# Kernel tuning notes

Measured on AMD Instinct MI355X. Metric: run time of the kernel, lower is better.

Reference implementation:

```python
import jax, jax.numpy as jnp
import numpy as np


def setup_inputs() -> dict:
    key = jax.random.key(0)
    k1, k2 = jax.random.split(key)
    video_feat = jax.random.normal(k1, (64, 1024, 512), dtype=jnp.float32)
    lang_feat = jax.random.normal(k2, (64, 512, 512), dtype=jnp.float32)
    return {"video_feat": video_feat, "lang_feat": lang_feat}


def _batch_pairwise_dist(x, y):
    # x: [B, Nv, D], y: [B, Nl, D] -> [B, Nv, Nl] squared-L2 (expanded form)
    a = jnp.sum(x * x, axis=2, keepdims=True)            # [B, Nv, 1]
    b = jnp.sum(y * y, axis=2, keepdims=True)            # [B, Nl, 1]
    ab = jnp.einsum('bvd,bld->bvl', x, y)                # [B, Nv, Nl]
    return a - 2.0 * ab + jnp.swapaxes(b, 1, 2)


def reference(video_feat, lang_feat):
    pairwise_dist = _batch_pairwise_dist(video_feat, lang_feat)  # [B, Nv, Nl]
    Nv = pairwise_dist.shape[1]
    Nl = pairwise_dist.shape[2]
    language_to_clip_dist = jnp.min(pairwise_dist, axis=2).sum(axis=1) / Nv
    clip_to_language_dist = jnp.min(pairwise_dist, axis=1).sum(axis=1) / Nl
    return language_to_clip_dist + clip_to_language_dist  # [B]
```

## Files before the change

kernel.cpp:

```cpp
#include <hip/hip_runtime.h>
#include <math.h>

#define BATCH 64
#define NV 1024
#define NL 512
#define DIM 512
#define TMM 256
#define TNN 256
#define BK 32
#define NKT (DIM / BK)

typedef __bf16 bf16x8 __attribute__((ext_vector_type(8)));
typedef __bf16 bf16x4 __attribute__((ext_vector_type(4)));
typedef float f32x4 __attribute__((ext_vector_type(4)));

__global__ __launch_bounds__(512, 2) void fused_distmin_kernel(
    const float* __restrict__ video, const float* __restrict__ lang,
    float* __restrict__ rowpart, float* __restrict__ colpart) {
    __shared__ __align__(16) ushort AsU[2][4][TMM][8];
    __shared__ __align__(16) ushort BsU[2][4][TNN][8];
    __shared__ float anrm[TMM], bnrm[TNN];
    float* rowred = (float*)AsU;
    float* colred = (float*)AsU + 2 * TMM;

    const int wg = ((blockIdx.x & 7) << 6) | (blockIdx.x >> 3);
    const int b = wg >> 3;
    const int mt = (wg >> 1) & 3;
    const int nt = wg & 1;

    const int tid = threadIdx.x;
    const int lane = tid & 63;
    const int w = tid >> 6;
    const int wrow = w >> 1;
    const int wcol = w & 1;
    const int lr = lane & 15;
    const int g = lane >> 4;

    const int half = tid & 1;
    const int o_sl = (tid >> 4) & 3;
    const int srow = ((tid >> 6) << 3) + ((tid >> 1) & 7);
    const int skq = o_sl * 2 + half;

    const float* Ath = video + ((size_t)b * NV + (size_t)mt * TMM + srow) * DIM + skq * 4;
    const float* Bth = lang + ((size_t)b * NL + (size_t)nt * TNN + srow) * DIM + skq * 4;

    float nA[4] = {0.f, 0.f, 0.f, 0.f};
    float nB[4] = {0.f, 0.f, 0.f, 0.f};

    f32x4 acc[4][8];
#pragma unroll
    for (int i = 0; i < 4; i++)
#pragma unroll
        for (int j = 0; j < 8; j++) acc[i][j] = (f32x4){0.f, 0.f, 0.f, 0.f};

    float4 va[4], vb[4];

    auto load_chunk = [&](int k0) {
#pragma unroll
        for (int t = 0; t < 4; ++t) {
            va[t] = *(const float4*)(Ath + (size_t)t * 64 * DIM + k0);
            vb[t] = *(const float4*)(Bth + (size_t)t * 64 * DIM + k0);
        }
    };
    auto write_chunk = [&](int buf) {
#pragma unroll
        for (int t = 0; t < 4; ++t) {
            float4 v = va[t];
            nA[t] += v.x * v.x + v.y * v.y + v.z * v.z + v.w * v.w;
            bf16x4 p = {(__bf16)v.x, (__bf16)v.y, (__bf16)v.z, (__bf16)v.w};
            *(bf16x4*)&AsU[buf][o_sl][srow + 64 * t][half * 4] = p;
            float4 u = vb[t];
            nB[t] += u.x * u.x + u.y * u.y + u.z * u.z + u.w * u.w;
            bf16x4 q = {(__bf16)u.x, (__bf16)u.y, (__bf16)u.z, (__bf16)u.w};
            *(bf16x4*)&BsU[buf][o_sl][srow + 64 * t][half * 4] = q;
        }
    };

    load_chunk(0);
    write_chunk(0);
    __syncthreads();

    for (int kt = 0; kt < NKT; ++kt) {
        const int cur = kt & 1;
        const bool more = (kt + 1) < NKT;
        if (more) load_chunk((kt + 1) * BK);

        bf16x8 av[4], bv[8];
#pragma unroll
        for (int fr = 0; fr < 4; ++fr)
            av[fr] = *(const bf16x8*)&AsU[cur][g][wrow * 64 + fr * 16 + lr][0];
#pragma unroll
        for (int fc = 0; fc < 8; ++fc)
            bv[fc] = *(const bf16x8*)&BsU[cur][g][wcol * 128 + fc * 16 + lr][0];
#pragma unroll
        for (int fr = 0; fr < 4; ++fr)
#pragma unroll
            for (int fc = 0; fc < 8; ++fc)
                acc[fr][fc] = __builtin_amdgcn_mfma_f32_16x16x32_bf16(
                    av[fr], bv[fc], acc[fr][fc], 0, 0, 0);

        if (more) write_chunk(cur ^ 1);
        __syncthreads();
    }

#pragma unroll
    for (int si = 0; si < 3; ++si) {
        const int s = (si == 0) ? 1 : (si == 1) ? 16 : 32;
#pragma unroll
        for (int t = 0; t < 4; ++t) {
            nA[t] += __shfl_xor(nA[t], s);
            nB[t] += __shfl_xor(nB[t], s);
        }
    }
    if ((tid & 49) == 0) {
#pragma unroll
        for (int t = 0; t < 4; ++t) {
            anrm[srow + 64 * t] = nA[t];
            bnrm[srow + 64 * t] = nB[t];
        }
    }
    __syncthreads();

    const int rgrp = (lane >> 4) * 4;
    float anorm[4][4];
#pragma unroll
    for (int fr = 0; fr < 4; ++fr)
#pragma unroll
        for (int r = 0; r < 4; ++r)
            anorm[fr][r] = anrm[wrow * 64 + fr * 16 + rgrp + r];
    float bnorm[8];
#pragma unroll
    for (int fc = 0; fc < 8; ++fc)
        bnorm[fc] = bnrm[wcol * 128 + fc * 16 + lr];

    float rmin[4][4];
    float cmin[8];
#pragma unroll
    for (int fr = 0; fr < 4; ++fr)
#pragma unroll
        for (int r = 0; r < 4; ++r) rmin[fr][r] = INFINITY;
#pragma unroll
    for (int fc = 0; fc < 8; ++fc) cmin[fc] = INFINITY;

#pragma unroll
    for (int fr = 0; fr < 4; ++fr)
#pragma unroll
        for (int fc = 0; fc < 8; ++fc)
#pragma unroll
            for (int r = 0; r < 4; ++r) {
                float d = anorm[fr][r] - 2.0f * acc[fr][fc][r] + bnorm[fc];
                rmin[fr][r] = fminf(rmin[fr][r], d);
                cmin[fc] = fminf(cmin[fc], d);
            }

#pragma unroll
    for (int fr = 0; fr < 4; ++fr)
#pragma unroll
        for (int r = 0; r < 4; ++r) {
#pragma unroll
            for (int off = 1; off < 16; off <<= 1)
                rmin[fr][r] = fminf(rmin[fr][r], __shfl_xor(rmin[fr][r], off));
        }
#pragma unroll
    for (int fc = 0; fc < 8; ++fc) {
#pragma unroll
        for (int off = 16; off < 64; off <<= 1)
            cmin[fc] = fminf(cmin[fc], __shfl_xor(cmin[fc], off));
    }

    if ((lane & 15) == 0) {
#pragma unroll
        for (int fr = 0; fr < 4; ++fr)
#pragma unroll
            for (int r = 0; r < 4; ++r)
                rowred[wcol * TMM + wrow * 64 + fr * 16 + rgrp + r] = rmin[fr][r];
    }
    if (lane < 16) {
#pragma unroll
        for (int fc = 0; fc < 8; ++fc)
            colred[wrow * TNN + wcol * 128 + fc * 16 + lane] = cmin[fc];
    }
    __syncthreads();
    if (tid < TMM) {
        rowpart[((size_t)(b * 2 + nt)) * NV + mt * TMM + tid] =
            fminf(rowred[tid], rowred[TMM + tid]);
    } else {
        int c2 = tid - TMM;
        float m = INFINITY;
#pragma unroll
        for (int k = 0; k < 4; ++k) m = fminf(m, colred[k * TNN + c2]);
        colpart[((size_t)(b * 4 + mt)) * NL + nt * TNN + c2] = m;
    }
}

__global__ __launch_bounds__(256) void reduce2_kernel(
    const float* __restrict__ rowpart, const float* __restrict__ colpart,
    float* __restrict__ out) {
    int b = blockIdx.x;
    int tid = threadIdx.x;
    float s = 0.0f;
    for (int r = tid; r < NV; r += 256) {
        float m = fminf(rowpart[((size_t)(b * 2 + 0)) * NV + r],
                        rowpart[((size_t)(b * 2 + 1)) * NV + r]);
        s += m * (1.0f / NV);
    }
    for (int c = tid; c < NL; c += 256) {
        float m = INFINITY;
#pragma unroll
        for (int mt = 0; mt < 4; mt++)
            m = fminf(m, colpart[((size_t)(b * 4 + mt)) * NL + c]);
        s += m * (1.0f / NL);
    }
    __shared__ float red[4];
#pragma unroll
    for (int off = 32; off > 0; off >>= 1) s += __shfl_down(s, off);
    if ((tid & 63) == 0) red[tid >> 6] = s;
    __syncthreads();
    if (tid == 0) out[b] = red[0] + red[1] + red[2] + red[3];
}

extern "C" void kernel_launch(void* const* d_in, const int* in_sizes, int n_in,
                              void* d_out, int out_size, void* d_ws, size_t ws_size,
                              hipStream_t stream) {
    const float* video = (const float*)d_in[0];
    const float* lang = (const float*)d_in[1];
    float* out = (float*)d_out;

    float* rowpart = (float*)d_ws;
    float* colpart = rowpart + (size_t)BATCH * 2 * NV;

    fused_distmin_kernel<<<dim3(512), 512, 0, stream>>>(video, lang, rowpart, colpart);
    reduce2_kernel<<<BATCH, 256, 0, stream>>>(rowpart, colpart, out);
}
```

Baseline: 66.45 us.

## Stream fp32 tiles into LDS via async global_load_lds with swizzled layout

Replaces the register-staged global loads and bf16 conversion before the LDS store with direct global-to-LDS async loads of raw fp32 data into an XOR-swizzled double buffer. Conversion to bf16 and the norm accumulation now happen after the LDS read, inside the MFMA loop, and are tracked with explicit vmcnt waits and barriers. The aim is to free registers and VALU work from the load path and overlap memory with compute. In exchange LDS footprint doubles because fp32 is stored, each wave converts redundantly, and per-iteration LDS traffic rises, which can hurt occupancy.

```diff
diff --git a/kernel.cpp b/kernel.cpp
--- a/kernel.cpp
+++ b/kernel.cpp
@@ -11,17 +11,22 @@
 #define NKT (DIM / BK)
 
 typedef __bf16 bf16x8 __attribute__((ext_vector_type(8)));
-typedef __bf16 bf16x4 __attribute__((ext_vector_type(4)));
 typedef float f32x4 __attribute__((ext_vector_type(4)));
+
+__device__ __forceinline__ void gload16(const void* g, void* lds) {
+    __builtin_amdgcn_global_load_lds((const __attribute__((address_space(1))) void*)g,
+                                     (__attribute__((address_space(3))) void*)lds,
+                                     16, 0, 0);
+}
 
 __global__ __launch_bounds__(512, 2) void fused_distmin_kernel(
     const float* __restrict__ video, const float* __restrict__ lang,
     float* __restrict__ rowpart, float* __restrict__ colpart) {
-    __shared__ __align__(16) ushort AsU[2][4][TMM][8];
-    __shared__ __align__(16) ushort BsU[2][4][TNN][8];
+    __shared__ __align__(16) char Abuf[2][TMM * BK * 4];
+    __shared__ __align__(16) char Bbuf[2][TNN * BK * 4];
     __shared__ float anrm[TMM], bnrm[TNN];
-    float* rowred = (float*)AsU;
-    float* colred = (float*)AsU + 2 * TMM;
+    float* rowred = (float*)Abuf;
+    float* colred = (float*)Abuf + 2 * TMM;
 
     const int wg = ((blockIdx.x & 7) << 6) | (blockIdx.x >> 3);
     const int b = wg >> 3;
@@ -35,17 +40,18 @@
     const int wcol = w & 1;
     const int lr = lane & 15;
     const int g = lane >> 4;
-
-    const int half = tid & 1;
-    const int o_sl = (tid >> 4) & 3;
-    const int srow = ((tid >> 6) << 3) + ((tid >> 1) & 7);
-    const int skq = o_sl * 2 + half;
-
-    const float* Ath = video + ((size_t)b * NV + (size_t)mt * TMM + srow) * DIM + skq * 4;
-    const float* Bth = lang + ((size_t)b * NL + (size_t)nt * TNN + srow) * DIM + skq * 4;
+    const int swz = (lr & 7) << 4;
+
+    const int srcRow = tid >> 3;
+    const int srcCb = (((tid >> 3) & 7) ^ (tid & 7)) << 4;
+    const char* aSrc = (const char*)video +
+        ((size_t)(b * NV + mt * TMM + srcRow)) * DIM * 4 + srcCb;
+    const char* bSrc = (const char*)lang +
+        ((size_t)(b * NL + nt * TNN + srcRow)) * DIM * 4 + srcCb;
+    const int dstOff = w * 1024;
 
     float nA[4] = {0.f, 0.f, 0.f, 0.f};
-    float nB[4] = {0.f, 0.f, 0.f, 0.f};
+    float nB[8] = {0.f, 0.f, 0.f, 0.f, 0.f, 0.f, 0.f, 0.f};
 
     f32x4 acc[4][8];
 #pragma unroll
@@ -53,71 +59,79 @@
 #pragma unroll
         for (int j = 0; j < 8; j++) acc[i][j] = (f32x4){0.f, 0.f, 0.f, 0.f};
 
-    float4 va[4], vb[4];
-
-    auto load_chunk = [&](int k0) {
-#pragma unroll
-        for (int t = 0; t < 4; ++t) {
-            va[t] = *(const float4*)(Ath + (size_t)t * 64 * DIM + k0);
-            vb[t] = *(const float4*)(Bth + (size_t)t * 64 * DIM + k0);
-        }
-    };
-    auto write_chunk = [&](int buf) {
-#pragma unroll
-        for (int t = 0; t < 4; ++t) {
-            float4 v = va[t];
-            nA[t] += v.x * v.x + v.y * v.y + v.z * v.z + v.w * v.w;
-            bf16x4 p = {(__bf16)v.x, (__bf16)v.y, (__bf16)v.z, (__bf16)v.w};
-            *(bf16x4*)&AsU[buf][o_sl][srow + 64 * t][half * 4] = p;
-            float4 u = vb[t];
-            nB[t] += u.x * u.x + u.y * u.y + u.z * u.z + u.w * u.w;
-            bf16x4 q = {(__bf16)u.x, (__bf16)u.y, (__bf16)u.z, (__bf16)u.w};
-            *(bf16x4*)&BsU[buf][o_sl][srow + 64 * t][half * 4] = q;
-        }
-    };
-
-    load_chunk(0);
-    write_chunk(0);
-    __syncthreads();
-
-    for (int kt = 0; kt < NKT; ++kt) {
-        const int cur = kt & 1;
-        const bool more = (kt + 1) < NKT;
-        if (more) load_chunk((kt + 1) * BK);
-
-        bf16x8 av[4], bv[8];
-#pragma unroll
-        for (int fr = 0; fr < 4; ++fr)
-            av[fr] = *(const bf16x8*)&AsU[cur][g][wrow * 64 + fr * 16 + lr][0];
-#pragma unroll
-        for (int fc = 0; fc < 8; ++fc)
-            bv[fc] = *(const bf16x8*)&BsU[cur][g][wcol * 128 + fc * 16 + lr][0];
-#pragma unroll
-        for (int fr = 0; fr < 4; ++fr)
-#pragma unroll
-            for (int fc = 0; fc < 8; ++fc)
-                acc[fr][fc] = __builtin_amdgcn_mfma_f32_16x16x32_bf16(
-                    av[fr], bv[fc], acc[fr][fc], 0, 0, 0);
-
-        if (more) write_chunk(cur ^ 1);
-        __syncthreads();
-    }
-
-#pragma unroll
-    for (int si = 0; si < 3; ++si) {
-        const int s = (si == 0) ? 1 : (si == 1) ? 16 : 32;
-#pragma unroll
-        for (int t = 0; t < 4; ++t) {
-            nA[t] += __shfl_xor(nA[t], s);
-            nB[t] += __shfl_xor(nB[t], s);
-        }
-    }
-    if ((tid & 49) == 0) {
-#pragma unroll
-        for (int t = 0; t < 4; ++t) {
-            anrm[srow + 64 * t] = nA[t];
-            bnrm[srow + 64 * t] = nB[t];
-        }
+#define ISSUE(BUF, KT)                                                        \
+    {                                                                         \
+        _Pragma("unroll") for (int t = 0; t < 4; ++t) {                       \
+            gload16(aSrc + (size_t)t * 64 * DIM * 4 + (size_t)(KT) * BK * 4,  \
+                    &Abuf[BUF][dstOff + t * 8192]);                           \
+            gload16(bSrc + (size_t)t * 64 * DIM * 4 + (size_t)(KT) * BK * 4,  \
+                    &Bbuf[BUF][dstOff + t * 8192]);                           \
+        }                                                                     \
+    }
+
+#define K_ITER(BUF, KISS, VMASM)                                              \
+    {                                                                         \
+        asm volatile(VMASM ::: "memory");                                     \
+        __builtin_amdgcn_s_barrier();                                         \
+        const char* Ab = Abuf[BUF];                                           \
+        const char* Bb = Bbuf[BUF];                                           \
+        bf16x8 av[4], bv[8];                                                  \
+        _Pragma("unroll") for (int fr = 0; fr < 4; ++fr) {                    \
+            const int row = wrow * 64 + fr * 16 + lr;                         \
+            float4 lo = *(const float4*)(Ab + row * 128 + ((g * 32) ^ swz));  \
+            float4 hi = *(const float4*)(Ab + row * 128 + ((g * 32 + 16) ^ swz)); \
+            if (wcol == 0)                                                    \
+                nA[fr] += lo.x * lo.x + lo.y * lo.y + lo.z * lo.z + lo.w * lo.w + \
+                          hi.x * hi.x + hi.y * hi.y + hi.z * hi.z + hi.w * hi.w; \
+            av[fr] = (bf16x8){(__bf16)lo.x, (__bf16)lo.y, (__bf16)lo.z, (__bf16)lo.w, \
+                              (__bf16)hi.x, (__bf16)hi.y, (__bf16)hi.z, (__bf16)hi.w}; \
+        }                                                                     \
+        _Pragma("unroll") for (int fc = 0; fc < 8; ++fc) {                    \
+            const int row = wcol * 128 + fc * 16 + lr;                        \
+            float4 lo = *(const float4*)(Bb + row * 128 + ((g * 32) ^ swz));  \
+            float4 hi = *(const float4*)(Bb + row * 128 + ((g * 32 + 16) ^ swz)); \
+            if (wrow == 0)                                                    \
+                nB[fc] += lo.x * lo.x + lo.y * lo.y + lo.z * lo.z + lo.w * lo.w + \
+                          hi.x * hi.x + hi.y * hi.y + hi.z * hi.z + hi.w * hi.w; \
+            bv[fc] = (bf16x8){(__bf16)lo.x, (__bf16)lo.y, (__bf16)lo.z, (__bf16)lo.w, \
+                              (__bf16)hi.x, (__bf16)hi.y, (__bf16)hi.z, (__bf16)hi.w}; \
+        }                                                                     \
+        asm volatile("s_waitcnt lgkmcnt(0)" ::: "memory");                    \
+        __builtin_amdgcn_s_barrier();                                         \
+        if ((KISS) >= 0) ISSUE(BUF, KISS);                                    \
+        _Pragma("unroll") for (int fr = 0; fr < 4; ++fr)                      \
+            _Pragma("unroll") for (int fc = 0; fc < 8; ++fc)                  \
+                acc[fr][fc] = __builtin_amdgcn_mfma_f32_16x16x32_bf16(        \
+                    av[fr], bv[fc], acc[fr][fc], 0, 0, 0);                    \
+    }
+
+    ISSUE(0, 0);
+    ISSUE(1, 1);
+
+    for (int kt = 0; kt < NKT - 2; kt += 2) {
+        K_ITER(0, kt + 2, "s_waitcnt vmcnt(8)");
+        K_ITER(1, kt + 3, "s_waitcnt vmcnt(8)");
+    }
+    K_ITER(0, -1, "s_waitcnt vmcnt(8)");
+    K_ITER(1, -1, "s_waitcnt vmcnt(0)");
+
+#pragma unroll
+    for (int fr = 0; fr < 4; ++fr) {
+        nA[fr] += __shfl_xor(nA[fr], 16);
+        nA[fr] += __shfl_xor(nA[fr], 32);
+    }
+#pragma unroll
+    for (int fc = 0; fc < 8; ++fc) {
+        nB[fc] += __shfl_xor(nB[fc], 16);
+        nB[fc] += __shfl_xor(nB[fc], 32);
+    }
+    if (wcol == 0 && lane < 16) {
+#pragma unroll
+        for (int fr = 0; fr < 4; ++fr) anrm[wrow * 64 + fr * 16 + lane] = nA[fr];
+    }
+    if (wrow == 0 && lane < 16) {
+#pragma unroll
+        for (int fc = 0; fc < 8; ++fc) bnrm[wcol * 128 + fc * 16 + lane] = nB[fc];
     }
     __syncthreads();
 
@@ -191,6 +205,8 @@
         for (int k = 0; k < 4; ++k) m = fminf(m, colred[k * TNN + c2]);
         colpart[((size_t)(b * 4 + mt)) * NL + nt * TNN + c2] = m;
     }
+#undef K_ITER
+#undef ISSUE
 }
 
 __global__ __launch_bounds__(256) void reduce2_kernel(
```

Measured after the change: 134.2 us. 102% more time.
